# Kernel tuning notes

Hardware: AMD Instinct MI355X
Metric: run time of the kernel (lower is better)

The kernel has to match this reference:

```python
import jax, jax.numpy as jnp
import numpy as np

TOP_K = 2          # n_activated_experts
ROUTE_SCALE = 1.0  # args.route_scale


def setup_inputs() -> dict:
    key = jax.random.key(0)
    ks = jax.random.split(key, 12)
    B, S, D, I, E = 8, 2048, 512, 1024, 8
    SH = 2 * I  # n_shared_experts * moe_inter_dim
    std = 0.02
    return {
        "x": jax.random.normal(ks[0], (B, S, D), jnp.float32),
        "gate_w": (jax.random.normal(ks[1], (E, D), jnp.float32) * std),
        "w1": (jax.random.normal(ks[2], (E, D, I), jnp.float32) * std),
        "w2": (jax.random.normal(ks[3], (E, I, D), jnp.float32) * std),
        "w3": (jax.random.normal(ks[4], (E, D, I), jnp.float32) * std),
        "sw1": (jax.random.normal(ks[5], (D, SH), jnp.float32) * std),
        "sb1": jnp.zeros((SH,), jnp.float32),
        "sw2": (jax.random.normal(ks[6], (SH, D), jnp.float32) * std),
        "sb2": jnp.zeros((D,), jnp.float32),
        "sw3": (jax.random.normal(ks[7], (D, SH), jnp.float32) * std),
        "sb3": jnp.zeros((SH,), jnp.float32),
    }


def reference(x, gate_w, w1, w2, w3, sw1, sb1, sw2, sb2, sw3, sb3):
    B, S, D = x.shape
    xt = x.reshape(-1, D)              # [T, D] tokens
    T = xt.shape[0]
    E = gate_w.shape[0]

    # --- Gate: sigmoid scores, top-k, renormalized weights ---
    scores = jax.nn.sigmoid(xt @ gate_w.T)                 # [T, E]
    topv, topi = jax.lax.top_k(scores, TOP_K)              # [T, K]
    wts = topv / jnp.sum(topv, axis=-1, keepdims=True)
    wts = wts * ROUTE_SCALE

    # Dense combine weights: zero for non-selected experts -> faithful to
    # the torch masked scatter-accumulate over the expert loop.
    cw = jnp.zeros((T, E), xt.dtype).at[jnp.arange(T)[:, None], topi].add(wts)

    # --- Routed SwiGLU experts (ffn_bias=False) ---
    y = jnp.zeros_like(xt)
    for e in range(E):  # fixed small structural loop over experts
        h = jax.nn.silu(xt @ w1[e]) * (xt @ w3[e])         # [T, I]
        y = y + cw[:, e:e + 1] * (h @ w2[e])               # combine

    # --- Load-balance aux loss L_ExpBal ---
    counts = jnp.zeros((E,), xt.dtype).at[topi.reshape(-1)].add(1.0)
    f_i = E * counts / (TOP_K * T)
    P_i = cw.sum(axis=0) / T   # per-expert sum of routed weights
    L_ExpBal = jnp.sum(f_i * P_i)

    # --- Shared experts MLP (biased Linear, SwiGLU) ---
    z = (jax.nn.silu(xt @ sw1 + sb1) * (xt @ sw3 + sb3)) @ sw2 + sb2

    return (y + z).reshape(B, S, D), L_ExpBal
```

## Files before the change

kernel.cpp:

```cpp
#include <hip/hip_runtime.h>
#include <math.h>
#include <stdint.h>

#define T_TOK 16384
#define DDIM  512
#define IDIM  1024
#define NEXP  8
#define SHDIM 2048
#define MT_R  264
#define MPAD  (MT_R * 128)
#define GBLK  256

typedef unsigned short u16;
typedef short bf16x8 __attribute__((ext_vector_type(8)));
typedef float f32x4 __attribute__((ext_vector_type(4)));

__device__ __forceinline__ u16 f2bf(float f) {
    unsigned u = __float_as_uint(f);
    u += 0x7FFF + ((u >> 16) & 1);
    return (u16)(u >> 16);
}

__device__ __forceinline__ void gload_lds16(const void* g, void* l) {
    __builtin_amdgcn_global_load_lds(
        (const __attribute__((address_space(1))) void*)g,
        (__attribute__((address_space(3))) void*)l, 16, 0, 0);
}

__global__ void k_zero(int* cursors) {
    int i = threadIdx.x;
    if (i < NEXP) cursors[i] = 0;
}

__global__ __launch_bounds__(256) void k_gate(
    const float* __restrict__ x, const float* __restrict__ gw,
    int* __restrict__ topi, float* __restrict__ wts,
    int* __restrict__ pcnt, float* __restrict__ pps, u16* __restrict__ xb)
{
    __shared__ int   cnt[NEXP];
    __shared__ float ps[NEXP];
    const int tid = threadIdx.x;
    if (tid < NEXP) { cnt[tid] = 0; ps[tid] = 0.f; }
    __syncthreads();
    const int wid = tid >> 6, lane = tid & 63;

    float gwr[DDIM / 64][NEXP];
#pragma unroll
    for (int j = 0; j < DDIM / 64; j++)
#pragma unroll
        for (int e = 0; e < NEXP; e++) gwr[j][e] = gw[e * DDIM + lane + 64 * j];

    const int t0 = blockIdx.x * 64 + wid * 16;
    for (int u = 0; u < 16; u++) {
        int t = t0 + u;
        const float* xr = x + (size_t)t * DDIM;
        float acc[NEXP];
#pragma unroll
        for (int e = 0; e < NEXP; e++) acc[e] = 0.f;
#pragma unroll
        for (int j = 0; j < DDIM / 64; j++) {
            float xv = xr[lane + 64 * j];
            xb[(size_t)t * DDIM + lane + 64 * j] = f2bf(xv);
#pragma unroll
            for (int e = 0; e < NEXP; e++) acc[e] += xv * gwr[j][e];
        }
#pragma unroll
        for (int e = 0; e < NEXP; e++) {
#pragma unroll
            for (int off = 32; off; off >>= 1) acc[e] += __shfl_xor(acc[e], off, 64);
        }
        if (lane == 0) {
            float s[NEXP];
#pragma unroll
            for (int e = 0; e < NEXP; e++) s[e] = 1.f / (1.f + expf(-acc[e]));
            int i1 = 0; float v1 = s[0];
#pragma unroll
            for (int e = 1; e < NEXP; e++) if (s[e] > v1) { v1 = s[e]; i1 = e; }
            int i2 = -1; float v2 = -1.f;
#pragma unroll
            for (int e = 0; e < NEXP; e++) if (e != i1 && s[e] > v2) { v2 = s[e]; i2 = e; }
            float inv = 1.f / (v1 + v2);
            float wa = v1 * inv, wb = v2 * inv;
            topi[2 * t] = i1; topi[2 * t + 1] = i2;
            wts[2 * t] = wa;  wts[2 * t + 1] = wb;
            atomicAdd(&cnt[i1], 1); atomicAdd(&cnt[i2], 1);
            atomicAdd(&ps[i1], wa); atomicAdd(&ps[i2], wb);
        }
    }
    __syncthreads();
    if (tid < NEXP) {
        pcnt[blockIdx.x * NEXP + tid] = cnt[tid];
        pps[blockIdx.x * NEXP + tid]  = ps[tid];
    }
}

__global__ void k_scan(const int* __restrict__ pcnt, const float* __restrict__ pps,
                       int* __restrict__ off_pad, float* __restrict__ out_loss)
{
    __shared__ int   scnt[8][NEXP];
    __shared__ float sps[8][NEXP];
    int tid = threadIdx.x;
    if (tid < 64) {
        int e = tid & 7, part = tid >> 3;
        int c = 0; float p = 0.f;
        for (int b = part * 32; b < part * 32 + 32; b++) {
            c += pcnt[b * NEXP + e];
            p += pps[b * NEXP + e];
        }
        scnt[part][e] = c; sps[part][e] = p;
    }
    __syncthreads();
    if (tid == 0) {
        int off = 0; float L = 0.f;
        for (int e = 0; e < NEXP; e++) {
            int c = 0; float p = 0.f;
            for (int q = 0; q < 8; q++) { c += scnt[q][e]; p += sps[q][e]; }
            off_pad[e] = off;
            off += (c + 127) & ~127;
            float f = (float)NEXP * (float)c / (float)(2 * T_TOK);
            L += f * (p / (float)T_TOK);
        }
        off_pad[NEXP] = off;
        out_loss[0] = L;
    }
}

__global__ void k_fillperm(int* __restrict__ perm) {
    int i = blockIdx.x * blockDim.x + threadIdx.x;
    if (i < MPAD) perm[i] = -1;
}

__global__ __launch_bounds__(256) void k_scatter(
    const int* __restrict__ topi, const float* __restrict__ wts,
    const int* __restrict__ off_pad, int* __restrict__ cursors,
    int* __restrict__ perm, float* __restrict__ pw)
{
    __shared__ int lcnt[NEXP];
    __shared__ int lbase[NEXP];
    int tid = threadIdx.x;
    if (tid < NEXP) lcnt[tid] = 0;
    __syncthreads();
    int t = blockIdx.x * 256 + tid;
    int e0 = topi[2 * t], e1 = topi[2 * t + 1];
    int p0 = atomicAdd(&lcnt[e0], 1);
    int p1 = atomicAdd(&lcnt[e1], 1);
    __syncthreads();
    if (tid < NEXP) lbase[tid] = atomicAdd(&cursors[tid], lcnt[tid]);
    __syncthreads();
    int s0 = off_pad[e0] + lbase[e0] + p0;
    int s1 = off_pad[e1] + lbase[e1] + p1;
    perm[s0] = t; pw[s0] = wts[2 * t];
    perm[s1] = t; pw[s1] = wts[2 * t + 1];
}

__global__ __launch_bounds__(256) void k_gather(const u16* __restrict__ xb,
                                                const int* __restrict__ perm,
                                                u16* __restrict__ xg) {
    int row = blockIdx.x * 2 + (threadIdx.x >> 7);
    int c = (threadIdx.x & 127) * 4;
    int tok = perm[row];
    ushort4 v = {0, 0, 0, 0};
    if (tok >= 0) v = *(const ushort4*)&xb[(size_t)tok * DDIM + c];
    *(ushort4*)&xg[(size_t)row * DDIM + c] = v;
}

__global__ __launch_bounds__(256) void k_transpose(const float* __restrict__ src,
                                                   u16* __restrict__ dst, int R, int C)
{
    __shared__ u16 t[64][68];
    const float* s = src + (size_t)blockIdx.z * R * C;
    u16* d = dst + (size_t)blockIdx.z * R * C;
    int r0 = blockIdx.y * 64, c0 = blockIdx.x * 64;
    int tid = threadIdx.x;
    int lr = tid >> 4, lc = (tid & 15) * 4;
#pragma unroll
    for (int u = 0; u < 4; u++) {
        int r = lr + u * 16;
        float4 v = *(const float4*)&s[(size_t)(r0 + r) * C + c0 + lc];
        t[lc + 0][r] = f2bf(v.x);
        t[lc + 1][r] = f2bf(v.y);
        t[lc + 2][r] = f2bf(v.z);
        t[lc + 3][r] = f2bf(v.w);
    }
    __syncthreads();
    int wr = tid >> 4, wc = (tid & 15) * 4;
#pragma unroll
    for (int u = 0; u < 4; u++) {
        int c = wr + u * 16;
        ushort4 o = { t[c][wc], t[c][wc + 1], t[c][wc + 2], t[c][wc + 3] };
        *(ushort4*)&d[(size_t)(c0 + c) * R + r0 + wc] = o;
    }
}

template<int K, bool ROUTED, bool BIAS>
__global__ __launch_bounds__(256, 2) void k_s1(
    const u16* __restrict__ A, const u16* __restrict__ B1t, const u16* __restrict__ B3t,
    const float* __restrict__ bias1, const float* __restrict__ bias3,
    u16* __restrict__ H, int ldh, const int* __restrict__ off_pad)
{
    __shared__ __align__(16) u16 sA[128 * 32], sB1[128 * 32], sB3[128 * 32];
    const int m0 = blockIdx.y * 128;
    if (ROUTED && m0 >= off_pad[NEXP]) return;
    const int n0 = blockIdx.x * 128;
    const u16* b1 = B1t; const u16* b3 = B3t;
    if (ROUTED) {
        int e = 0;
        while (off_pad[e + 1] <= m0) e++;
        b1 += (size_t)e * IDIM * DDIM;
        b3 += (size_t)e * IDIM * DDIM;
    }
    const int tid = threadIdx.x;
    const int wid = tid >> 6, lane = tid & 63;
    const int srow = wid * 16 + (lane >> 2);
    const int skk  = (lane & 3) * 8;
    const u16* gA  = A  + (size_t)(m0 + srow) * K + skk;
    const u16* gB1 = b1 + (size_t)(n0 + srow) * K + skk;
    const u16* gB3 = b3 + (size_t)(n0 + srow) * K + skk;
    u16* lA  = sA  + wid * 512;
    u16* lB1 = sB1 + wid * 512;
    u16* lB3 = sB3 + wid * 512;
    const int fr = lane & 15;
    const int fk = (lane >> 4) * 8;
    const int wrow = (wid >> 1) * 64, wcol = (wid & 1) * 64;

    f32x4 acc1[4][4], acc3[4][4];
#pragma unroll
    for (int i = 0; i < 4; i++)
#pragma unroll
        for (int j = 0; j < 4; j++) { acc1[i][j] = {0.f, 0.f, 0.f, 0.f}; acc3[i][j] = {0.f, 0.f, 0.f, 0.f}; }

    for (int k0 = 0; k0 < K; k0 += 32) {
#pragma unroll
        for (int p = 0; p < 2; p++) {
            gload_lds16(gA  + (size_t)p * 64 * K + k0, lA  + p * 2048);
            gload_lds16(gB1 + (size_t)p * 64 * K + k0, lB1 + p * 2048);
            gload_lds16(gB3 + (size_t)p * 64 * K + k0, lB3 + p * 2048);
        }
        __syncthreads();
        bf16x8 av[4], b1v[4], b3v[4];
#pragma unroll
        for (int i = 0; i < 4; i++) {
            av[i]  = *(const bf16x8*)(sA  + (wrow + i * 16 + fr) * 32 + fk);
            b1v[i] = *(const bf16x8*)(sB1 + (wcol + i * 16 + fr) * 32 + fk);
            b3v[i] = *(const bf16x8*)(sB3 + (wcol + i * 16 + fr) * 32 + fk);
        }
#pragma unroll
        for (int i = 0; i < 4; i++)
#pragma unroll
            for (int j = 0; j < 4; j++) {
                acc1[i][j] = __builtin_amdgcn_mfma_f32_16x16x32_bf16(av[i], b1v[j], acc1[i][j], 0, 0, 0);
                acc3[i][j] = __builtin_amdgcn_mfma_f32_16x16x32_bf16(av[i], b3v[j], acc3[i][j], 0, 0, 0);
            }
        __syncthreads();
    }

    const int rr = (lane >> 4) * 4;
#pragma unroll
    for (int i = 0; i < 4; i++) {
#pragma unroll
        for (int j = 0; j < 4; j++) {
            int col = n0 + wcol + j * 16 + fr;
            float bb1 = BIAS ? bias1[col] : 0.f;
            float bb3 = BIAS ? bias3[col] : 0.f;
#pragma unroll
            for (int r = 0; r < 4; r++) {
                int row = m0 + wrow + i * 16 + rr + r;
                float v1 = acc1[i][j][r] + bb1;
                float v3 = acc3[i][j][r] + bb3;
                float hv = (v1 / (1.f + __expf(-v1))) * v3;
                H[(size_t)row * ldh + col] = f2bf(hv);
            }
        }
    }
}

template<int K, bool ROUTED>
__global__ __launch_bounds__(256, 2) void k_s2(
    const u16* __restrict__ A, const u16* __restrict__ Bt,
    const float* __restrict__ bias2, float* __restrict__ out,
    const int* __restrict__ off_pad, const int* __restrict__ perm,
    const float* __restrict__ pw)
{
    __shared__ __align__(16) u16 sA[128 * 32], sB[128 * 32];
    const int m0 = blockIdx.y * 128;
    if (ROUTED && m0 >= off_pad[NEXP]) return;
    const int n0 = blockIdx.x * 128;
    const u16* bt = Bt;
    if (ROUTED) {
        int e = 0;
        while (off_pad[e + 1] <= m0) e++;
        bt += (size_t)e * DDIM * IDIM;
    }
    const int tid = threadIdx.x;
    const int wid = tid >> 6, lane = tid & 63;
    const int srow = wid * 16 + (lane >> 2);
    const int skk  = (lane & 3) * 8;
    const u16* gA = A  + (size_t)(m0 + srow) * K + skk;
    const u16* gB = bt + (size_t)(n0 + srow) * K + skk;
    u16* lA = sA + wid * 512;
    u16* lB = sB + wid * 512;
    const int fr = lane & 15;
    const int fk = (lane >> 4) * 8;
    const int wrow = (wid >> 1) * 64, wcol = (wid & 1) * 64;

    f32x4 acc[4][4];
#pragma unroll
    for (int i = 0; i < 4; i++)
#pragma unroll
        for (int j = 0; j < 4; j++) acc[i][j] = {0.f, 0.f, 0.f, 0.f};

    for (int k0 = 0; k0 < K; k0 += 32) {
#pragma unroll
        for (int p = 0; p < 2; p++) {
            gload_lds16(gA + (size_t)p * 64 * K + k0, lA + p * 2048);
            gload_lds16(gB + (size_t)p * 64 * K + k0, lB + p * 2048);
        }
        __syncthreads();
        bf16x8 av[4], bv[4];
#pragma unroll
        for (int i = 0; i < 4; i++) {
            av[i] = *(const bf16x8*)(sA + (wrow + i * 16 + fr) * 32 + fk);
            bv[i] = *(const bf16x8*)(sB + (wcol + i * 16 + fr) * 32 + fk);
        }
#pragma unroll
        for (int i = 0; i < 4; i++)
#pragma unroll
            for (int j = 0; j < 4; j++)
                acc[i][j] = __builtin_amdgcn_mfma_f32_16x16x32_bf16(av[i], bv[j], acc[i][j], 0, 0, 0);
        __syncthreads();
    }

    const int rr = (lane >> 4) * 4;
#pragma unroll
    for (int i = 0; i < 4; i++) {
#pragma unroll
        for (int r = 0; r < 4; r++) {
            int row = m0 + wrow + i * 16 + rr + r;
            int tok = ROUTED ? perm[row] : row;
            float sc = ROUTED ? ((tok >= 0) ? pw[row] : 0.f) : 1.f;
#pragma unroll
            for (int j = 0; j < 4; j++) {
                int col = n0 + wcol + j * 16 + fr;
                float v = acc[i][j][r];
                if (ROUTED) {
                    if (tok >= 0) atomicAdd(&out[(size_t)tok * DDIM + col], sc * v);
                } else {
                    out[(size_t)row * DDIM + col] = v + bias2[col];
                }
            }
        }
    }
}

extern "C" void kernel_launch(void* const* d_in, const int* in_sizes, int n_in,
                              void* d_out, int out_size, void* d_ws, size_t ws_size,
                              hipStream_t stream)
{
    const float* x   = (const float*)d_in[0];
    const float* gw  = (const float*)d_in[1];
    const float* w1  = (const float*)d_in[2];
    const float* w2  = (const float*)d_in[3];
    const float* w3  = (const float*)d_in[4];
    const float* sw1 = (const float*)d_in[5];
    const float* sb1 = (const float*)d_in[6];
    const float* sw2 = (const float*)d_in[7];
    const float* sb2 = (const float*)d_in[8];
    const float* sw3 = (const float*)d_in[9];
    const float* sb3 = (const float*)d_in[10];
    float* out = (float*)d_out;

    char* ws = (char*)d_ws;
    size_t off = 0;
    int*   topi    = (int*)(ws + off);   off += (size_t)2 * T_TOK * 4;
    float* wts     = (float*)(ws + off); off += (size_t)2 * T_TOK * 4;
    int*   perm    = (int*)(ws + off);   off += (size_t)MPAD * 4;
    float* pw      = (float*)(ws + off); off += (size_t)MPAD * 4;
    int*   cursors = (int*)(ws + off);   off += 256;
    int*   off_pad = (int*)(ws + off);   off += 256;
    int*   pcnt    = (int*)(ws + off);   off += (size_t)GBLK * NEXP * 4;
    float* pps     = (float*)(ws + off); off += (size_t)GBLK * NEXP * 4;
    u16*   xb      = (u16*)(ws + off);   off += (size_t)T_TOK * DDIM * 2;
    u16*   xg      = (u16*)(ws + off);   off += (size_t)MPAD * DDIM * 2;
    u16*   w1T     = (u16*)(ws + off);   off += (size_t)NEXP * IDIM * DDIM * 2;
    u16*   w3T     = (u16*)(ws + off);   off += (size_t)NEXP * IDIM * DDIM * 2;
    u16*   w2T     = (u16*)(ws + off);   off += (size_t)NEXP * DDIM * IDIM * 2;
    u16*   sw1T    = (u16*)(ws + off);   off += (size_t)SHDIM * DDIM * 2;
    u16*   sw3T    = (u16*)(ws + off);   off += (size_t)SHDIM * DDIM * 2;
    u16*   sw2T    = (u16*)(ws + off);   off += (size_t)DDIM * SHDIM * 2;
    u16*   hb      = (u16*)(ws + off);   off += (size_t)MPAD * IDIM * 2;

    k_zero<<<1, 64, 0, stream>>>(cursors);
    k_gate<<<GBLK, 256, 0, stream>>>(x, gw, topi, wts, pcnt, pps, xb);
    k_scan<<<1, 64, 0, stream>>>(pcnt, pps, off_pad, out + (size_t)T_TOK * DDIM);
    k_fillperm<<<(MPAD + 255) / 256, 256, 0, stream>>>(perm);
    k_scatter<<<T_TOK / 256, 256, 0, stream>>>(topi, wts, off_pad, cursors, perm, pw);

    k_gather<<<MPAD / 2, 256, 0, stream>>>(xb, perm, xg);
    k_transpose<<<dim3(IDIM / 64, DDIM / 64, NEXP), 256, 0, stream>>>(w1, w1T, DDIM, IDIM);
    k_transpose<<<dim3(IDIM / 64, DDIM / 64, NEXP), 256, 0, stream>>>(w3, w3T, DDIM, IDIM);
    k_transpose<<<dim3(DDIM / 64, IDIM / 64, NEXP), 256, 0, stream>>>(w2, w2T, IDIM, DDIM);
    k_transpose<<<dim3(SHDIM / 64, DDIM / 64, 1), 256, 0, stream>>>(sw1, sw1T, DDIM, SHDIM);
    k_transpose<<<dim3(SHDIM / 64, DDIM / 64, 1), 256, 0, stream>>>(sw3, sw3T, DDIM, SHDIM);
    k_transpose<<<dim3(DDIM / 64, SHDIM / 64, 1), 256, 0, stream>>>(sw2, sw2T, SHDIM, DDIM);

    k_s1<DDIM, false, true><<<dim3(SHDIM / 128, T_TOK / 128), 256, 0, stream>>>(
        xb, sw1T, sw3T, sb1, sb3, hb, SHDIM, nullptr);
    k_s2<SHDIM, false><<<dim3(DDIM / 128, T_TOK / 128), 256, 0, stream>>>(
        hb, sw2T, sb2, out, nullptr, nullptr, nullptr);
    k_s1<DDIM, true, false><<<dim3(IDIM / 128, MT_R), 256, 0, stream>>>(
        xg, w1T, w3T, nullptr, nullptr, hb, IDIM, off_pad);
    k_s2<IDIM, true><<<dim3(DDIM / 128, MT_R), 256, 0, stream>>>(
        hb, w2T, nullptr, out, off_pad, perm, pw);
}
```

Measured before the change: 432.6 us.

## Double-buffer GEMM LDS loads, swizzle blocks across XCDs, replace atomic combine

The two GEMM kernels now use double-buffered LDS tiles, so the next k-slice is prefetched while the current one feeds MFMA. Workgroup IDs are remapped across the XCDs for better L2 locality. The routed second GEMM no longer does scattered fp32 atomicAdds into the output. It writes bf16 rows to a temp buffer, and a new combine kernel gathers each token's two expert rows through an inverse permutation and adds them. The gate kernel is also vectorised with float4 loads. This costs an extra pass over the output plus a bf16 rounding of the routed partial results.

```diff
diff --git a/kernel.cpp b/kernel.cpp
--- a/kernel.cpp
+++ b/kernel.cpp
@@ -20,6 +20,9 @@
     u += 0x7FFF + ((u >> 16) & 1);
     return (u16)(u >> 16);
 }
+__device__ __forceinline__ float bf2f(u16 h) {
+    return __uint_as_float((unsigned)h << 16);
+}
 
 __device__ __forceinline__ void gload_lds16(const void* g, void* l) {
     __builtin_amdgcn_global_load_lds(
@@ -27,6 +30,10 @@
         (__attribute__((address_space(3))) void*)l, 16, 0, 0);
 }
 
+__device__ __forceinline__ int xcd_swz(int id, int nwg) {
+    return (id & 7) * (nwg >> 3) + (id >> 3);
+}
+
 __global__ void k_zero(int* cursors) {
     int i = threadIdx.x;
     if (i < NEXP) cursors[i] = 0;
@@ -44,25 +51,30 @@
     __syncthreads();
     const int wid = tid >> 6, lane = tid & 63;
 
-    float gwr[DDIM / 64][NEXP];
-#pragma unroll
-    for (int j = 0; j < DDIM / 64; j++)
-#pragma unroll
-        for (int e = 0; e < NEXP; e++) gwr[j][e] = gw[e * DDIM + lane + 64 * j];
+    const float4* gw4 = (const float4*)gw;
+    float4 g0[NEXP], g1[NEXP];
+#pragma unroll
+    for (int e = 0; e < NEXP; e++) {
+        g0[e] = gw4[e * 128 + lane];
+        g1[e] = gw4[e * 128 + 64 + lane];
+    }
 
     const int t0 = blockIdx.x * 64 + wid * 16;
     for (int u = 0; u < 16; u++) {
         int t = t0 + u;
-        const float* xr = x + (size_t)t * DDIM;
+        const float4* xr4 = (const float4*)(x + (size_t)t * DDIM);
+        float4 v0 = xr4[lane];
+        float4 v1 = xr4[64 + lane];
+        ushort4 o0 = { f2bf(v0.x), f2bf(v0.y), f2bf(v0.z), f2bf(v0.w) };
+        ushort4 o1 = { f2bf(v1.x), f2bf(v1.y), f2bf(v1.z), f2bf(v1.w) };
+        ushort4* xbo = (ushort4*)(xb + (size_t)t * DDIM);
+        xbo[lane] = o0;
+        xbo[64 + lane] = o1;
         float acc[NEXP];
 #pragma unroll
-        for (int e = 0; e < NEXP; e++) acc[e] = 0.f;
-#pragma unroll
-        for (int j = 0; j < DDIM / 64; j++) {
-            float xv = xr[lane + 64 * j];
-            xb[(size_t)t * DDIM + lane + 64 * j] = f2bf(xv);
-#pragma unroll
-            for (int e = 0; e < NEXP; e++) acc[e] += xv * gwr[j][e];
+        for (int e = 0; e < NEXP; e++) {
+            acc[e] = v0.x * g0[e].x + v0.y * g0[e].y + v0.z * g0[e].z + v0.w * g0[e].w
+                   + v1.x * g1[e].x + v1.y * g1[e].y + v1.z * g1[e].z + v1.w * g1[e].w;
         }
 #pragma unroll
         for (int e = 0; e < NEXP; e++) {
@@ -73,14 +85,14 @@
             float s[NEXP];
 #pragma unroll
             for (int e = 0; e < NEXP; e++) s[e] = 1.f / (1.f + expf(-acc[e]));
-            int i1 = 0; float v1 = s[0];
-#pragma unroll
-            for (int e = 1; e < NEXP; e++) if (s[e] > v1) { v1 = s[e]; i1 = e; }
-            int i2 = -1; float v2 = -1.f;
-#pragma unroll
-            for (int e = 0; e < NEXP; e++) if (e != i1 && s[e] > v2) { v2 = s[e]; i2 = e; }
-            float inv = 1.f / (v1 + v2);
-            float wa = v1 * inv, wb = v2 * inv;
+            int i1 = 0; float v1s = s[0];
+#pragma unroll
+            for (int e = 1; e < NEXP; e++) if (s[e] > v1s) { v1s = s[e]; i1 = e; }
+            int i2 = -1; float v2s = -1.f;
+#pragma unroll
+            for (int e = 0; e < NEXP; e++) if (e != i1 && s[e] > v2s) { v2s = s[e]; i2 = e; }
+            float inv = 1.f / (v1s + v2s);
+            float wa = v1s * inv, wb = v2s * inv;
             topi[2 * t] = i1; topi[2 * t + 1] = i2;
             wts[2 * t] = wa;  wts[2 * t + 1] = wb;
             atomicAdd(&cnt[i1], 1); atomicAdd(&cnt[i2], 1);
@@ -133,7 +145,7 @@
 __global__ __launch_bounds__(256) void k_scatter(
     const int* __restrict__ topi, const float* __restrict__ wts,
     const int* __restrict__ off_pad, int* __restrict__ cursors,
-    int* __restrict__ perm, float* __restrict__ pw)
+    int* __restrict__ perm, float* __restrict__ pw, int* __restrict__ inv)
 {
     __shared__ int lcnt[NEXP];
     __shared__ int lbase[NEXP];
@@ -151,6 +163,7 @@
     int s1 = off_pad[e1] + lbase[e1] + p1;
     perm[s0] = t; pw[s0] = wts[2 * t];
     perm[s1] = t; pw[s1] = wts[2 * t + 1];
+    inv[2 * t] = s0; inv[2 * t + 1] = s1;
 }
 
 __global__ __launch_bounds__(256) void k_gather(const u16* __restrict__ xb,
@@ -198,10 +211,12 @@
     const float* __restrict__ bias1, const float* __restrict__ bias3,
     u16* __restrict__ H, int ldh, const int* __restrict__ off_pad)
 {
-    __shared__ __align__(16) u16 sA[128 * 32], sB1[128 * 32], sB3[128 * 32];
-    const int m0 = blockIdx.y * 128;
+    __shared__ __align__(16) u16 sA[2][128 * 32], sB1[2][128 * 32], sB3[2][128 * 32];
+    const int nwg = gridDim.x * gridDim.y;
+    const int id  = xcd_swz(blockIdx.y * gridDim.x + blockIdx.x, nwg);
+    const int m0 = (id / gridDim.x) * 128;
+    const int n0 = (id % gridDim.x) * 128;
     if (ROUTED && m0 >= off_pad[NEXP]) return;
-    const int n0 = blockIdx.x * 128;
     const u16* b1 = B1t; const u16* b3 = B3t;
     if (ROUTED) {
         int e = 0;
@@ -216,9 +231,7 @@
     const u16* gA  = A  + (size_t)(m0 + srow) * K + skk;
     const u16* gB1 = b1 + (size_t)(n0 + srow) * K + skk;
     const u16* gB3 = b3 + (size_t)(n0 + srow) * K + skk;
-    u16* lA  = sA  + wid * 512;
-    u16* lB1 = sB1 + wid * 512;
-    u16* lB3 = sB3 + wid * 512;
+    const int ldst = wid * 512;
     const int fr = lane & 15;
     const int fk = (lane >> 4) * 8;
     const int wrow = (wid >> 1) * 64, wcol = (wid & 1) * 64;
@@ -229,20 +242,30 @@
 #pragma unroll
         for (int j = 0; j < 4; j++) { acc1[i][j] = {0.f, 0.f, 0.f, 0.f}; acc3[i][j] = {0.f, 0.f, 0.f, 0.f}; }
 
+#pragma unroll
+    for (int p = 0; p < 2; p++) {
+        gload_lds16(gA  + (size_t)p * 64 * K, &sA [0][ldst + p * 2048]);
+        gload_lds16(gB1 + (size_t)p * 64 * K, &sB1[0][ldst + p * 2048]);
+        gload_lds16(gB3 + (size_t)p * 64 * K, &sB3[0][ldst + p * 2048]);
+    }
+    __syncthreads();
+
+    int cur = 0;
     for (int k0 = 0; k0 < K; k0 += 32) {
-#pragma unroll
-        for (int p = 0; p < 2; p++) {
-            gload_lds16(gA  + (size_t)p * 64 * K + k0, lA  + p * 2048);
-            gload_lds16(gB1 + (size_t)p * 64 * K + k0, lB1 + p * 2048);
-            gload_lds16(gB3 + (size_t)p * 64 * K + k0, lB3 + p * 2048);
-        }
-        __syncthreads();
+        if (k0 + 32 < K) {
+#pragma unroll
+            for (int p = 0; p < 2; p++) {
+                gload_lds16(gA  + (size_t)p * 64 * K + k0 + 32, &sA [cur ^ 1][ldst + p * 2048]);
+                gload_lds16(gB1 + (size_t)p * 64 * K + k0 + 32, &sB1[cur ^ 1][ldst + p * 2048]);
+                gload_lds16(gB3 + (size_t)p * 64 * K + k0 + 32, &sB3[cur ^ 1][ldst + p * 2048]);
+            }
+        }
         bf16x8 av[4], b1v[4], b3v[4];
 #pragma unroll
         for (int i = 0; i < 4; i++) {
-            av[i]  = *(const bf16x8*)(sA  + (wrow + i * 16 + fr) * 32 + fk);
-            b1v[i] = *(const bf16x8*)(sB1 + (wcol + i * 16 + fr) * 32 + fk);
-            b3v[i] = *(const bf16x8*)(sB3 + (wcol + i * 16 + fr) * 32 + fk);
+            av[i]  = *(const bf16x8*)(&sA [cur][(wrow + i * 16 + fr) * 32 + fk]);
+            b1v[i] = *(const bf16x8*)(&sB1[cur][(wcol + i * 16 + fr) * 32 + fk]);
+            b3v[i] = *(const bf16x8*)(&sB3[cur][(wcol + i * 16 + fr) * 32 + fk]);
         }
 #pragma unroll
         for (int i = 0; i < 4; i++)
@@ -252,6 +275,7 @@
                 acc3[i][j] = __builtin_amdgcn_mfma_f32_16x16x32_bf16(av[i], b3v[j], acc3[i][j], 0, 0, 0);
             }
         __syncthreads();
+        cur ^= 1;
     }
 
     const int rr = (lane >> 4) * 4;
@@ -278,13 +302,14 @@
 __global__ __launch_bounds__(256, 2) void k_s2(
     const u16* __restrict__ A, const u16* __restrict__ Bt,
     const float* __restrict__ bias2, float* __restrict__ out,
-    const int* __restrict__ off_pad, const int* __restrict__ perm,
-    const float* __restrict__ pw)
-{
-    __shared__ __align__(16) u16 sA[128 * 32], sB[128 * 32];
-    const int m0 = blockIdx.y * 128;
+    u16* __restrict__ ytmp, const int* __restrict__ off_pad)
+{
+    __shared__ __align__(16) u16 sA[2][128 * 32], sB[2][128 * 32];
+    const int nwg = gridDim.x * gridDim.y;
+    const int id  = xcd_swz(blockIdx.y * gridDim.x + blockIdx.x, nwg);
+    const int m0 = (id / gridDim.x) * 128;
+    const int n0 = (id % gridDim.x) * 128;
     if (ROUTED && m0 >= off_pad[NEXP]) return;
-    const int n0 = blockIdx.x * 128;
     const u16* bt = Bt;
     if (ROUTED) {
         int e = 0;
@@ -297,8 +322,7 @@
     const int skk  = (lane & 3) * 8;
     const u16* gA = A  + (size_t)(m0 + srow) * K + skk;
     const u16* gB = bt + (size_t)(n0 + srow) * K + skk;
-    u16* lA = sA + wid * 512;
-    u16* lB = sB + wid * 512;
+    const int ldst = wid * 512;
     const int fr = lane & 15;
     const int fk = (lane >> 4) * 8;
     const int wrow = (wid >> 1) * 64, wcol = (wid & 1) * 64;
@@ -309,18 +333,27 @@
 #pragma unroll
         for (int j = 0; j < 4; j++) acc[i][j] = {0.f, 0.f, 0.f, 0.f};
 
+#pragma unroll
+    for (int p = 0; p < 2; p++) {
+        gload_lds16(gA + (size_t)p * 64 * K, &sA[0][ldst + p * 2048]);
+        gload_lds16(gB + (size_t)p * 64 * K, &sB[0][ldst + p * 2048]);
+    }
+    __syncthreads();
+
+    int cur = 0;
     for (int k0 = 0; k0 < K; k0 += 32) {
-#pragma unroll
-        for (int p = 0; p < 2; p++) {
-            gload_lds16(gA + (size_t)p * 64 * K + k0, lA + p * 2048);
-            gload_lds16(gB + (size_t)p * 64 * K + k0, lB + p * 2048);
-        }
-        __syncthreads();
+        if (k0 + 32 < K) {
+#pragma unroll
+            for (int p = 0; p < 2; p++) {
+                gload_lds16(gA + (size_t)p * 64 * K + k0 + 32, &sA[cur ^ 1][ldst + p * 2048]);
+                gload_lds16(gB + (size_t)p * 64 * K + k0 + 32, &sB[cur ^ 1][ldst + p * 2048]);
+            }
+        }
         bf16x8 av[4], bv[4];
 #pragma unroll
         for (int i = 0; i < 4; i++) {
-            av[i] = *(const bf16x8*)(sA + (wrow + i * 16 + fr) * 32 + fk);
-            bv[i] = *(const bf16x8*)(sB + (wcol + i * 16 + fr) * 32 + fk);
+            av[i] = *(const bf16x8*)(&sA[cur][(wrow + i * 16 + fr) * 32 + fk]);
+            bv[i] = *(const bf16x8*)(&sB[cur][(wcol + i * 16 + fr) * 32 + fk]);
         }
 #pragma unroll
         for (int i = 0; i < 4; i++)
@@ -328,6 +361,7 @@
             for (int j = 0; j < 4; j++)
                 acc[i][j] = __builtin_amdgcn_mfma_f32_16x16x32_bf16(av[i], bv[j], acc[i][j], 0, 0, 0);
         __syncthreads();
+        cur ^= 1;
     }
 
     const int rr = (lane >> 4) * 4;
@@ -336,20 +370,37 @@
 #pragma unroll
         for (int r = 0; r < 4; r++) {
             int row = m0 + wrow + i * 16 + rr + r;
-            int tok = ROUTED ? perm[row] : row;
-            float sc = ROUTED ? ((tok >= 0) ? pw[row] : 0.f) : 1.f;
 #pragma unroll
             for (int j = 0; j < 4; j++) {
                 int col = n0 + wcol + j * 16 + fr;
                 float v = acc[i][j][r];
                 if (ROUTED) {
-                    if (tok >= 0) atomicAdd(&out[(size_t)tok * DDIM + col], sc * v);
+                    ytmp[(size_t)row * DDIM + col] = f2bf(v);
                 } else {
                     out[(size_t)row * DDIM + col] = v + bias2[col];
                 }
             }
         }
     }
+}
+
+__global__ __launch_bounds__(256) void k_combine(
+    const u16* __restrict__ ytmp, const int* __restrict__ inv,
+    const float* __restrict__ wts, float* __restrict__ out)
+{
+    int idx = blockIdx.x * 256 + threadIdx.x;
+    int t = idx >> 7;
+    int c = (idx & 127) * 4;
+    int s0 = inv[2 * t], s1 = inv[2 * t + 1];
+    float w0 = wts[2 * t], w1 = wts[2 * t + 1];
+    ushort4 a = *(const ushort4*)&ytmp[(size_t)s0 * DDIM + c];
+    ushort4 b = *(const ushort4*)&ytmp[(size_t)s1 * DDIM + c];
+    float4 o = *(float4*)&out[(size_t)t * DDIM + c];
+    o.x += w0 * bf2f(a.x) + w1 * bf2f(b.x);
+    o.y += w0 * bf2f(a.y) + w1 * bf2f(b.y);
+    o.z += w0 * bf2f(a.z) + w1 * bf2f(b.z);
+    o.w += w0 * bf2f(a.w) + w1 * bf2f(b.w);
+    *(float4*)&out[(size_t)t * DDIM + c] = o;
 }
 
 extern "C" void kernel_launch(void* const* d_in, const int* in_sizes, int n_in,
@@ -379,6 +430,7 @@
     int*   off_pad = (int*)(ws + off);   off += 256;
     int*   pcnt    = (int*)(ws + off);   off += (size_t)GBLK * NEXP * 4;
     float* pps     = (float*)(ws + off); off += (size_t)GBLK * NEXP * 4;
+    int*   inv     = (int*)(ws + off);   off += (size_t)2 * T_TOK * 4;
     u16*   xb      = (u16*)(ws + off);   off += (size_t)T_TOK * DDIM * 2;
     u16*   xg      = (u16*)(ws + off);   off += (size_t)MPAD * DDIM * 2;
     u16*   w1T     = (u16*)(ws + off);   off += (size_t)NEXP * IDIM * DDIM * 2;
@@ -388,12 +440,13 @@
     u16*   sw3T    = (u16*)(ws + off);   off += (size_t)SHDIM * DDIM * 2;
     u16*   sw2T    = (u16*)(ws + off);   off += (size_t)DDIM * SHDIM * 2;
     u16*   hb      = (u16*)(ws + off);   off += (size_t)MPAD * IDIM * 2;
+    u16*   ytmp    = xg;
 
     k_zero<<<1, 64, 0, stream>>>(cursors);
     k_gate<<<GBLK, 256, 0, stream>>>(x, gw, topi, wts, pcnt, pps, xb);
     k_scan<<<1, 64, 0, stream>>>(pcnt, pps, off_pad, out + (size_t)T_TOK * DDIM);
     k_fillperm<<<(MPAD + 255) / 256, 256, 0, stream>>>(perm);
-    k_scatter<<<T_TOK / 256, 256, 0, stream>>>(topi, wts, off_pad, cursors, perm, pw);
+    k_scatter<<<T_TOK / 256, 256, 0, stream>>>(topi, wts, off_pad, cursors, perm, pw, inv);
 
     k_gather<<<MPAD / 2, 256, 0, stream>>>(xb, perm, xg);
     k_transpose<<<dim3(IDIM / 64, DDIM / 64, NEXP), 256, 0, stream>>>(w1, w1T, DDIM, IDIM);
@@ -406,9 +459,10 @@
     k_s1<DDIM, false, true><<<dim3(SHDIM / 128, T_TOK / 128), 256, 0, stream>>>(
         xb, sw1T, sw3T, sb1, sb3, hb, SHDIM, nullptr);
     k_s2<SHDIM, false><<<dim3(DDIM / 128, T_TOK / 128), 256, 0, stream>>>(
-        hb, sw2T, sb2, out, nullptr, nullptr, nullptr);
+        hb, sw2T, sb2, out, nullptr, nullptr);
     k_s1<DDIM, true, false><<<dim3(IDIM / 128, MT_R), 256, 0, stream>>>(
         xg, w1T, w3T, nullptr, nullptr, hb, IDIM, off_pad);
     k_s2<IDIM, true><<<dim3(DDIM / 128, MT_R), 256, 0, stream>>>(
-        hb, w2T, nullptr, out, off_pad, perm, pw);
-}
+        hb, w2T, nullptr, nullptr, ytmp, off_pad);
+    k_combine<<<(T_TOK * DDIM / 4) / 256, 256, 0, stream>>>(ytmp, inv, wts, out);
+}
```

Result: faster. 387.2 us (-10.5%).
